# Kernel tuning notes

Measured on AMD Instinct MI355X. Metric: run time of the kernel, lower is better.

The kernel has to match this reference:

```python
import jax, jax.numpy as jnp
import numpy as np

N_HEAD = 16

def _apply_rotary(x, cos, sin):
    # x: (B,H,T,D); faithful to torch: x*cos + cat([-x[...,1::2], x[...,::2]], -1)*sin
    rot = jnp.concatenate([-x[..., 1::2], x[..., ::2]], axis=-1)
    return x * cos + rot * sin

def setup_inputs() -> dict:
    key = jax.random.key(0)
    k1, k2, k3 = jax.random.split(key, 3)
    B, T, C = 8, 1024, 1024
    x = jax.random.normal(k1, (B, T, C), dtype=jnp.float32)
    # scale weights like typical init to keep activations sane
    W_attn = jax.random.normal(k2, (3 * C, C), dtype=jnp.float32) * (C ** -0.5)
    W_proj = jax.random.normal(k3, (C, C), dtype=jnp.float32) * (C ** -0.5)
    return {"x": x, "W_attn": W_attn, "W_proj": W_proj}

def reference(x, W_attn, W_proj):
    B, T, C = x.shape
    H = N_HEAD
    D = C // H
    qkv = x @ W_attn.T                      # (B,T,3C)
    q, k, v = jnp.split(qkv, 3, axis=2)
    # (B,T,C) -> (B,H,T,D)
    def to_heads(t):
        return t.reshape(B, T, H, D).transpose(0, 2, 1, 3)
    q, k, v = to_heads(q), to_heads(k), to_heads(v)
    # Rotary module in source computes cos/sin of q itself (faithful reproduction)
    cos = jnp.cos(q)
    sin = jnp.sin(q)
    q = _apply_rotary(q, cos, sin)
    k = _apply_rotary(k, cos, sin)
    # causal attention, softmax_scale = 1.0 (as in the flash call)
    scores = jnp.einsum('bhqd,bhkd->bhqk', q, k)
    causal = jnp.tril(jnp.ones((T, T), dtype=bool))
    scores = jnp.where(causal, scores, jnp.finfo(scores.dtype).min)
    att = jax.nn.softmax(scores, axis=-1)
    y = jnp.einsum('bhqk,bhkd->bhqd', att, v)   # (B,H,T,D)
    y = y.transpose(0, 2, 1, 3).reshape(B, T, C)
    return y @ W_proj.T
```

## Files before the change

### kernel.cpp

```cpp
#include <hip/hip_runtime.h>

typedef __attribute__((ext_vector_type(8))) short v8s;
typedef __attribute__((ext_vector_type(8))) _Float16 f16x8;
typedef __attribute__((ext_vector_type(4))) _Float16 f16x4;
typedef __attribute__((ext_vector_type(4))) float f32x4;
typedef unsigned short u16;

#define MFMAH(a,b,c) __builtin_amdgcn_mfma_f32_16x16x32_f16((a),(b),(c),0,0,0)
#define L2E 1.4426950408889634f

__device__ __forceinline__ u16 f2h(float f) {
    _Float16 h = (_Float16)f;
    return __builtin_bit_cast(u16, h);
}

__device__ __forceinline__ void gload16(const u16* g, u16* l) {
    __builtin_amdgcn_global_load_lds((const __attribute__((address_space(1))) void*)g,
                                     (__attribute__((address_space(3))) void*)l, 16, 0, 0);
}

__device__ __forceinline__ void stage_tile(const u16* __restrict__ base, u16* lds, int w, int lane) {
    const int rsub = lane >> 3;
    const int s_org = (lane & 7) ^ rsub;
#pragma unroll
    for (int i = 0; i < 4; ++i) {
        const u16* src = base + (size_t)(32 * w + 8 * i + rsub) * 1024 + 8 * s_org;
        gload16(src, lds + (32 * w + 8 * i) * 64);
    }
}

__global__ __launch_bounds__(256) void split16_kernel(const float* __restrict__ in,
                                                      u16* __restrict__ hi, u16* __restrict__ lo, int n4) {
    int i = blockIdx.x * 256 + threadIdx.x;
    if (i >= n4) return;
    f32x4 v = ((const f32x4*)in)[i];
    f16x4 h, l;
#pragma unroll
    for (int j = 0; j < 4; ++j) {
        _Float16 hh = (_Float16)v[j];
        h[j] = hh;
        l[j] = (_Float16)(v[j] - (float)hh);
    }
    ((f16x4*)hi)[i] = h;
    ((f16x4*)lo)[i] = l;
}

__global__ __launch_bounds__(256) void cvt16_kernel(const float* __restrict__ in, u16* __restrict__ out, int n4) {
    int i = blockIdx.x * 256 + threadIdx.x;
    if (i >= n4) return;
    f32x4 v = ((const f32x4*)in)[i];
    f16x4 h;
#pragma unroll
    for (int j = 0; j < 4; ++j) h[j] = (_Float16)v[j];
    ((f16x4*)out)[i] = h;
}

__global__ __launch_bounds__(256) void qkv_gemm2(const u16* __restrict__ xh, const u16* __restrict__ xl,
                                                 const u16* __restrict__ wf, float* __restrict__ qkv) {
    __shared__ u16 sAh[8192], sAl[8192], sB[8192];
    const int bid = blockIdx.x;
    const int swz = (bid & 7) * 192 + (bid >> 3);
    const int mb = swz / 24, nb = swz % 24;
    const int m0 = mb * 128, n0 = nb * 128;
    const bool lo = (nb < 16);
    const int tid = threadIdx.x, lane = tid & 63, w = tid >> 6;
    const int wr = w >> 1, wc = w & 1;
    const int fr = lane & 15, fq = lane >> 4;
    const u16* pa = xh + (size_t)m0 * 1024;
    const u16* pal = xl + (size_t)m0 * 1024;
    const u16* pb = wf + (size_t)n0 * 1024;
    f32x4 acc[4][4] = {};
    for (int k0 = 0; k0 < 1024; k0 += 64) {
        stage_tile(pa + k0, sAh, w, lane);
        stage_tile(pb + k0, sB, w, lane);
        if (lo) stage_tile(pal + k0, sAl, w, lane);
        __syncthreads();
#pragma unroll
        for (int kk = 0; kk < 2; ++kk) {
            f16x8 ah[4], al[4], bb[4];
#pragma unroll
            for (int m = 0; m < 4; ++m) {
                int row = wr * 64 + m * 16 + fr;
                int off = row * 64 + ((((kk * 4 + fq)) ^ (fr & 7)) << 3);
                ah[m] = *(const f16x8*)&sAh[off];
                if (lo) al[m] = *(const f16x8*)&sAl[off];
            }
#pragma unroll
            for (int n = 0; n < 4; ++n) {
                int row = wc * 64 + n * 16 + fr;
                bb[n] = *(const f16x8*)&sB[row * 64 + ((((kk * 4 + fq)) ^ (fr & 7)) << 3)];
            }
#pragma unroll
            for (int n = 0; n < 4; ++n)
#pragma unroll
                for (int m = 0; m < 4; ++m) {
                    acc[m][n] = MFMAH(ah[m], bb[n], acc[m][n]);
                    if (lo) acc[m][n] = MFMAH(al[m], bb[n], acc[m][n]);
                }
        }
        __syncthreads();
    }
#pragma unroll
    for (int m = 0; m < 4; ++m) {
        int rowb = m0 + wr * 64 + m * 16 + fq * 4;
#pragma unroll
        for (int n = 0; n < 4; ++n) {
            int col = n0 + wc * 64 + n * 16 + fr;
#pragma unroll
            for (int r = 0; r < 4; ++r)
                qkv[(size_t)(rowb + r) * 3072 + col] = acc[m][n][r];
        }
    }
}

__global__ __launch_bounds__(256) void rotary_kernel(const float* __restrict__ qkv,
                                                     u16* __restrict__ qf, u16* __restrict__ kf,
                                                     u16* __restrict__ vt) {
    int rid = blockIdx.x * 4 + (threadIdx.x >> 6);
    int lane = threadIdx.x & 63;
    int b = rid >> 14, h = (rid >> 10) & 15, t = rid & 1023;
    const float* base = qkv + (size_t)(b * 1024 + t) * 3072 + h * 64 + lane;
    float q = base[0], k = base[1024], v = base[2048];
    float s, c;
    sincosf(q, &s, &c);
    int src = (lane < 32) ? (2 * lane + 1) : (2 * lane - 64);
    float qp = __shfl(q, src);
    float kp = __shfl(k, src);
    float rq = (lane < 32) ? -qp : qp;
    float rk = (lane < 32) ? -kp : kp;
    float q2 = q * c + rq * s;
    float k2 = k * c + rk * s;
    size_t oi = (size_t)((b * 16 + h) * 1024 + t) * 64 + lane;
    qf[oi] = f2h(q2);
    kf[oi] = f2h(k2);
    vt[(size_t)((b * 16 + h) * 64 + lane) * 1024 + t] = f2h(v);
}

__global__ __launch_bounds__(256) void attn_kernel(const u16* __restrict__ qf, const u16* __restrict__ kf,
                                                   const u16* __restrict__ vt, u16* __restrict__ yb) {
    __shared__ u16 sQ[4096], sK[4096], sV[4096], sP[4096];
    const int bh = blockIdx.x >> 4, qt = blockIdx.x & 15;
    const int b = bh >> 4, h = bh & 15;
    const int tid = threadIdx.x, lane = tid & 63, w = tid >> 6;
    const int q0 = qt * 64;
    const int fr = lane & 15, fq = lane >> 4;
    const int srow = tid >> 2, sc = (tid & 3) << 4;
    const int ss0 = sc >> 3;
    const int wr0 = srow * 64 + (((ss0    ) ^ (srow & 7)) << 3);
    const int wr1 = srow * 64 + (((ss0 + 1) ^ (srow & 7)) << 3);
    {
        const u16* g = qf + (size_t)(bh * 1024 + q0 + srow) * 64 + sc;
        *(v8s*)&sQ[wr0] = *(const v8s*)g;
        *(v8s*)&sQ[wr1] = *(const v8s*)(g + 8);
    }
    __syncthreads();
    f16x8 qfr[2];
    {
        int row = w * 16 + fr;
#pragma unroll
        for (int kk = 0; kk < 2; ++kk) {
            int sl = kk * 4 + fq;
            qfr[kk] = *(const f16x8*)&sQ[row * 64 + ((sl ^ (row & 7)) << 3)];
        }
    }
    f32x4 accy[4] = {};
    float m_r[4], l_r[4];
#pragma unroll
    for (int r = 0; r < 4; ++r) { m_r[r] = -1e30f; l_r[r] = 0.f; }
    const u16* gk = kf + (size_t)bh * 65536 + srow * 64 + sc;
    const u16* gv = vt + (size_t)(bh * 64 + srow) * 1024 + sc;

    for (int kt = 0; kt <= qt; ++kt) {
        __syncthreads();
        {
            const u16* a  = gk + kt * 4096;
            const u16* vg = gv + kt * 64;
            *(v8s*)&sK[wr0] = *(const v8s*)a;
            *(v8s*)&sK[wr1] = *(const v8s*)(a + 8);
            *(v8s*)&sV[wr0] = *(const v8s*)vg;
            *(v8s*)&sV[wr1] = *(const v8s*)(vg + 8);
        }
        __syncthreads();
        f32x4 s[4] = {};
#pragma unroll
        for (int n = 0; n < 4; ++n) {
            int krow = n * 16 + fr;
#pragma unroll
            for (int kk = 0; kk < 2; ++kk) {
                int sl = kk * 4 + fq;
                f16x8 kb = *(const f16x8*)&sK[krow * 64 + ((sl ^ (krow & 7)) << 3)];
                s[n] = MFMAH(qfr[kk], kb, s[n]);
            }
        }
        if (kt == qt) {
            int rowb = w * 16 + fq * 4;
#pragma unroll
            for (int n = 0; n < 4; ++n)
#pragma unroll
                for (int r = 0; r < 4; ++r)
                    if (n * 16 + fr > rowb + r) s[n][r] = -1e30f;
        }
        float alpha[4];
#pragma unroll
        for (int r = 0; r < 4; ++r) {
            float mx = fmaxf(fmaxf(s[0][r], s[1][r]), fmaxf(s[2][r], s[3][r]));
            mx = fmaxf(mx, __shfl_xor(mx, 1));
            mx = fmaxf(mx, __shfl_xor(mx, 2));
            mx = fmaxf(mx, __shfl_xor(mx, 4));
            mx = fmaxf(mx, __shfl_xor(mx, 8));
            float mn = fmaxf(m_r[r], mx);
            alpha[r] = exp2f((m_r[r] - mn) * L2E);
            m_r[r] = mn;
            float rs = 0.f;
#pragma unroll
            for (int n = 0; n < 4; ++n) {
                float p = exp2f((s[n][r] - mn) * L2E);
                s[n][r] = p;
                rs += p;
            }
            rs += __shfl_xor(rs, 1);
            rs += __shfl_xor(rs, 2);
            rs += __shfl_xor(rs, 4);
            rs += __shfl_xor(rs, 8);
            l_r[r] = l_r[r] * alpha[r] + rs;
        }
#pragma unroll
        for (int dn = 0; dn < 4; ++dn)
#pragma unroll
            for (int r = 0; r < 4; ++r) accy[dn][r] *= alpha[r];
        {
            int rowb = w * 16 + fq * 4;
#pragma unroll
            for (int n = 0; n < 4; ++n) {
                int key = n * 16 + fr;
                int s8 = key >> 3, kr = key & 7;
#pragma unroll
                for (int r = 0; r < 4; ++r) {
                    int row = rowb + r;
                    sP[row * 64 + (((s8 ^ (row & 7)) << 3) | kr)] = f2h(s[n][r]);
                }
            }
        }
        f16x8 pa[2];
        {
            int prow = w * 16 + fr;
#pragma unroll
            for (int kk = 0; kk < 2; ++kk) {
                int sl = kk * 4 + fq;
                pa[kk] = *(const f16x8*)&sP[prow * 64 + ((sl ^ (prow & 7)) << 3)];
            }
        }
#pragma unroll
        for (int dn = 0; dn < 4; ++dn) {
            int vrow = dn * 16 + fr;
#pragma unroll
            for (int kk = 0; kk < 2; ++kk) {
                int sl = kk * 4 + fq;
                f16x8 vb = *(const f16x8*)&sV[vrow * 64 + ((sl ^ (vrow & 7)) << 3)];
                accy[dn] = MFMAH(pa[kk], vb, accy[dn]);
            }
        }
    }
    {
        int rowb = q0 + w * 16 + fq * 4;
        int colb = h * 64 + fr;
#pragma unroll
        for (int r = 0; r < 4; ++r) {
            float inv = 1.0f / l_r[r];
#pragma unroll
            for (int dn = 0; dn < 4; ++dn)
                yb[(size_t)(b * 1024 + rowb + r) * 1024 + colb + dn * 16] = f2h(accy[dn][r] * inv);
        }
    }
}

__global__ __launch_bounds__(256) void proj_gemm2(const u16* __restrict__ yb, const u16* __restrict__ wpb,
                                                  float* __restrict__ out) {
    __shared__ u16 sA[8192], sB[8192];
    const int bid = blockIdx.x;
    const int swz = (bid & 7) * 64 + (bid >> 3);
    const int mb = swz >> 3, nb = swz & 7;
    const int m0 = mb * 128, n0 = nb * 128;
    const int tid = threadIdx.x, lane = tid & 63, w = tid >> 6;
    const int wr = w >> 1, wc = w & 1;
    const int fr = lane & 15, fq = lane >> 4;
    const u16* pa = yb + (size_t)m0 * 1024;
    const u16* pb = wpb + (size_t)n0 * 1024;
    f32x4 acc[4][4] = {};
    for (int k0 = 0; k0 < 1024; k0 += 64) {
        stage_tile(pa + k0, sA, w, lane);
        stage_tile(pb + k0, sB, w, lane);
        __syncthreads();
#pragma unroll
        for (int kk = 0; kk < 2; ++kk) {
            f16x8 af[4], bb[4];
#pragma unroll
            for (int m = 0; m < 4; ++m) {
                int row = wr * 64 + m * 16 + fr;
                af[m] = *(const f16x8*)&sA[row * 64 + ((((kk * 4 + fq)) ^ (fr & 7)) << 3)];
            }
#pragma unroll
            for (int n = 0; n < 4; ++n) {
                int row = wc * 64 + n * 16 + fr;
                bb[n] = *(const f16x8*)&sB[row * 64 + ((((kk * 4 + fq)) ^ (fr & 7)) << 3)];
            }
#pragma unroll
            for (int n = 0; n < 4; ++n)
#pragma unroll
                for (int m = 0; m < 4; ++m) acc[m][n] = MFMAH(af[m], bb[n], acc[m][n]);
        }
        __syncthreads();
    }
#pragma unroll
    for (int m = 0; m < 4; ++m) {
        int rowb = m0 + wr * 64 + m * 16 + fq * 4;
#pragma unroll
        for (int n = 0; n < 4; ++n) {
            int col = n0 + wc * 64 + n * 16 + fr;
#pragma unroll
            for (int r = 0; r < 4; ++r) out[(size_t)(rowb + r) * 1024 + col] = acc[m][n][r];
        }
    }
}

extern "C" void kernel_launch(void* const* d_in, const int* in_sizes, int n_in,
                              void* d_out, int out_size, void* d_ws, size_t ws_size,
                              hipStream_t stream) {
    const float* x  = (const float*)d_in[0];
    const float* Wa = (const float*)d_in[1];
    const float* Wp = (const float*)d_in[2];
    float* out = (float*)d_out;
    char* ws = (char*)d_ws;
    size_t off = 0;
    float* qkv = (float*)(ws + off); off += (size_t)8192 * 3072 * 4;
    u16* xh  = (u16*)(ws + off); off += 16777216;
    u16* xl  = (u16*)(ws + off); off += 16777216;
    u16* wf  = (u16*)(ws + off); off += 6291456;
    u16* wpb = (u16*)(ws + off); off += 2097152;
    u16* qf  = (u16*)(ws + off); off += 16777216;
    u16* kf  = (u16*)(ws + off); off += 16777216;
    u16* vt  = (u16*)(ws + off); off += 16777216;
    u16* yb  = (u16*)(ws + off); off += 16777216;

    split16_kernel<<<8192, 256, 0, stream>>>(x, xh, xl, 8192 * 1024 / 4);
    cvt16_kernel<<<3072, 256, 0, stream>>>(Wa, wf, 3072 * 1024 / 4);
    cvt16_kernel<<<1024, 256, 0, stream>>>(Wp, wpb, 1024 * 1024 / 4);
    qkv_gemm2<<<1536, 256, 0, stream>>>(xh, xl, wf, qkv);
    rotary_kernel<<<32768, 256, 0, stream>>>(qkv, qf, kf, vt);
    attn_kernel<<<2048, 256, 0, stream>>>(qf, kf, vt, yb);
    proj_gemm2<<<512, 256, 0, stream>>>(yb, wpb, out);
}
```

Measured before the change: 375.3 us.

## Pair causal query tiles per block to balance work and share K/V tiles

The attention kernel now gives each block two query tiles (qt and 15-qt), so every block runs the same number of key-tile iterations and each staged K/V tile serves both query tiles. Staging switches to async global_load_lds with a swizzled layout, the Q/P buffers are merged to cut shared memory, and launch bounds request 4 blocks per CU. The aim is to remove the load imbalance of the causal triangle and halve K/V reloads. In exchange the grid shrinks to 1024 blocks, the serial chain per block gets longer, and register pressure rises from two sets of accumulators.

```diff
diff --git a/kernel.cpp b/kernel.cpp
--- a/kernel.cpp
+++ b/kernel.cpp
@@ -26,6 +26,17 @@
     for (int i = 0; i < 4; ++i) {
         const u16* src = base + (size_t)(32 * w + 8 * i + rsub) * 1024 + 8 * s_org;
         gload16(src, lds + (32 * w + 8 * i) * 64);
+    }
+}
+
+__device__ __forceinline__ void stage64(const u16* __restrict__ base, size_t rstride,
+                                        u16* lds, int w, int lane) {
+    const int rsub = lane >> 3;
+    const int s_org = (lane & 7) ^ rsub;
+#pragma unroll
+    for (int i = 0; i < 2; ++i) {
+        const u16* src = base + (size_t)(16 * w + 8 * i + rsub) * rstride + 8 * s_org;
+        gload16(src, lds + (16 * w + 8 * i) * 64);
     }
 }
 
@@ -136,140 +147,144 @@
     vt[(size_t)((b * 16 + h) * 64 + lane) * 1024 + t] = f2h(v);
 }
 
-__global__ __launch_bounds__(256) void attn_kernel(const u16* __restrict__ qf, const u16* __restrict__ kf,
-                                                   const u16* __restrict__ vt, u16* __restrict__ yb) {
-    __shared__ u16 sQ[4096], sK[4096], sV[4096], sP[4096];
-    const int bh = blockIdx.x >> 4, qt = blockIdx.x & 15;
+__device__ __forceinline__ void attn_step(const f16x8* qfr, f32x4* accy, float* m_r, float* l_r,
+                                          const u16* sK, const u16* sV, u16* sP,
+                                          bool diag, int w, int lane) {
+    const int fr = lane & 15, fq = lane >> 4;
+    f32x4 s[4] = {};
+#pragma unroll
+    for (int n = 0; n < 4; ++n) {
+        int krow = n * 16 + fr;
+#pragma unroll
+        for (int kk = 0; kk < 2; ++kk) {
+            int sl = kk * 4 + fq;
+            f16x8 kb = *(const f16x8*)&sK[krow * 64 + ((sl ^ (krow & 7)) << 3)];
+            s[n] = MFMAH(qfr[kk], kb, s[n]);
+        }
+    }
+    if (diag) {
+        int rowb = w * 16 + fq * 4;
+#pragma unroll
+        for (int n = 0; n < 4; ++n)
+#pragma unroll
+            for (int r = 0; r < 4; ++r)
+                if (n * 16 + fr > rowb + r) s[n][r] = -1e30f;
+    }
+    float alpha[4];
+#pragma unroll
+    for (int r = 0; r < 4; ++r) {
+        float mx = fmaxf(fmaxf(s[0][r], s[1][r]), fmaxf(s[2][r], s[3][r]));
+        mx = fmaxf(mx, __shfl_xor(mx, 1));
+        mx = fmaxf(mx, __shfl_xor(mx, 2));
+        mx = fmaxf(mx, __shfl_xor(mx, 4));
+        mx = fmaxf(mx, __shfl_xor(mx, 8));
+        float mn = fmaxf(m_r[r], mx);
+        alpha[r] = exp2f((m_r[r] - mn) * L2E);
+        m_r[r] = mn;
+        float rs = 0.f;
+#pragma unroll
+        for (int n = 0; n < 4; ++n) {
+            float p = exp2f((s[n][r] - mn) * L2E);
+            s[n][r] = p;
+            rs += p;
+        }
+        rs += __shfl_xor(rs, 1);
+        rs += __shfl_xor(rs, 2);
+        rs += __shfl_xor(rs, 4);
+        rs += __shfl_xor(rs, 8);
+        l_r[r] = l_r[r] * alpha[r] + rs;
+    }
+#pragma unroll
+    for (int dn = 0; dn < 4; ++dn)
+#pragma unroll
+        for (int r = 0; r < 4; ++r) accy[dn][r] *= alpha[r];
+    {
+        int rowb = w * 16 + fq * 4;
+#pragma unroll
+        for (int n = 0; n < 4; ++n) {
+            int key = n * 16 + fr;
+            int s8 = key >> 3, kr = key & 7;
+#pragma unroll
+            for (int r = 0; r < 4; ++r) {
+                int row = rowb + r;
+                sP[row * 64 + (((s8 ^ (row & 7)) << 3) | kr)] = f2h(s[n][r]);
+            }
+        }
+    }
+    f16x8 pa[2];
+    {
+        int prow = w * 16 + fr;
+#pragma unroll
+        for (int kk = 0; kk < 2; ++kk) {
+            int sl = kk * 4 + fq;
+            pa[kk] = *(const f16x8*)&sP[prow * 64 + ((sl ^ (prow & 7)) << 3)];
+        }
+    }
+#pragma unroll
+    for (int dn = 0; dn < 4; ++dn) {
+        int vrow = dn * 16 + fr;
+#pragma unroll
+        for (int kk = 0; kk < 2; ++kk) {
+            int sl = kk * 4 + fq;
+            f16x8 vb = *(const f16x8*)&sV[vrow * 64 + ((sl ^ (vrow & 7)) << 3)];
+            accy[dn] = MFMAH(pa[kk], vb, accy[dn]);
+        }
+    }
+}
+
+__global__ __launch_bounds__(256, 4) void attn2_kernel(const u16* __restrict__ qf, const u16* __restrict__ kf,
+                                                       const u16* __restrict__ vt, u16* __restrict__ yb) {
+    __shared__ u16 sK[4096], sV[4096], sQP[4096];
+    const int bh = blockIdx.x >> 3, slot = blockIdx.x & 7;
     const int b = bh >> 4, h = bh & 15;
+    const int qtA = 15 - slot, qtB = slot;
     const int tid = threadIdx.x, lane = tid & 63, w = tid >> 6;
-    const int q0 = qt * 64;
     const int fr = lane & 15, fq = lane >> 4;
-    const int srow = tid >> 2, sc = (tid & 3) << 4;
-    const int ss0 = sc >> 3;
-    const int wr0 = srow * 64 + (((ss0    ) ^ (srow & 7)) << 3);
-    const int wr1 = srow * 64 + (((ss0 + 1) ^ (srow & 7)) << 3);
-    {
-        const u16* g = qf + (size_t)(bh * 1024 + q0 + srow) * 64 + sc;
-        *(v8s*)&sQ[wr0] = *(const v8s*)g;
-        *(v8s*)&sQ[wr1] = *(const v8s*)(g + 8);
-    }
+
+    stage64(qf + (size_t)bh * 65536 + qtA * 4096, 64, sK, w, lane);
+    stage64(qf + (size_t)bh * 65536 + qtB * 4096, 64, sV, w, lane);
     __syncthreads();
-    f16x8 qfr[2];
+    f16x8 qfrA[2], qfrB[2];
     {
         int row = w * 16 + fr;
 #pragma unroll
         for (int kk = 0; kk < 2; ++kk) {
             int sl = kk * 4 + fq;
-            qfr[kk] = *(const f16x8*)&sQ[row * 64 + ((sl ^ (row & 7)) << 3)];
-        }
-    }
-    f32x4 accy[4] = {};
-    float m_r[4], l_r[4];
-#pragma unroll
-    for (int r = 0; r < 4; ++r) { m_r[r] = -1e30f; l_r[r] = 0.f; }
-    const u16* gk = kf + (size_t)bh * 65536 + srow * 64 + sc;
-    const u16* gv = vt + (size_t)(bh * 64 + srow) * 1024 + sc;
-
-    for (int kt = 0; kt <= qt; ++kt) {
-        __syncthreads();
-        {
-            const u16* a  = gk + kt * 4096;
-            const u16* vg = gv + kt * 64;
-            *(v8s*)&sK[wr0] = *(const v8s*)a;
-            *(v8s*)&sK[wr1] = *(const v8s*)(a + 8);
-            *(v8s*)&sV[wr0] = *(const v8s*)vg;
-            *(v8s*)&sV[wr1] = *(const v8s*)(vg + 8);
-        }
-        __syncthreads();
-        f32x4 s[4] = {};
-#pragma unroll
-        for (int n = 0; n < 4; ++n) {
-            int krow = n * 16 + fr;
-#pragma unroll
-            for (int kk = 0; kk < 2; ++kk) {
-                int sl = kk * 4 + fq;
-                f16x8 kb = *(const f16x8*)&sK[krow * 64 + ((sl ^ (krow & 7)) << 3)];
-                s[n] = MFMAH(qfr[kk], kb, s[n]);
-            }
-        }
-        if (kt == qt) {
-            int rowb = w * 16 + fq * 4;
-#pragma unroll
-            for (int n = 0; n < 4; ++n)
-#pragma unroll
-                for (int r = 0; r < 4; ++r)
-                    if (n * 16 + fr > rowb + r) s[n][r] = -1e30f;
-        }
-        float alpha[4];
+            int off = row * 64 + ((sl ^ (row & 7)) << 3);
+            qfrA[kk] = *(const f16x8*)&sK[off];
+            qfrB[kk] = *(const f16x8*)&sV[off];
+        }
+    }
+    f32x4 accyA[4] = {}, accyB[4] = {};
+    float mA[4], lA[4], mB[4], lB[4];
+#pragma unroll
+    for (int r = 0; r < 4; ++r) { mA[r] = mB[r] = -1e30f; lA[r] = lB[r] = 0.f; }
+    const u16* kbase = kf + (size_t)bh * 65536;
+    const u16* vbase = vt + (size_t)bh * 65536;
+
+    for (int kt = 0; kt <= qtA; ++kt) {
+        __syncthreads();
+        stage64(kbase + kt * 4096, 64, sK, w, lane);
+        stage64(vbase + kt * 64, 1024, sV, w, lane);
+        __syncthreads();
+        attn_step(qfrA, accyA, mA, lA, sK, sV, sQP, kt == qtA, w, lane);
+        if (kt <= qtB)
+            attn_step(qfrB, accyB, mB, lB, sK, sV, sQP, kt == qtB, w, lane);
+    }
+    {
+        int rowbase = w * 16 + fq * 4;
+        int colb = h * 64 + fr;
 #pragma unroll
         for (int r = 0; r < 4; ++r) {
-            float mx = fmaxf(fmaxf(s[0][r], s[1][r]), fmaxf(s[2][r], s[3][r]));
-            mx = fmaxf(mx, __shfl_xor(mx, 1));
-            mx = fmaxf(mx, __shfl_xor(mx, 2));
-            mx = fmaxf(mx, __shfl_xor(mx, 4));
-            mx = fmaxf(mx, __shfl_xor(mx, 8));
-            float mn = fmaxf(m_r[r], mx);
-            alpha[r] = exp2f((m_r[r] - mn) * L2E);
-            m_r[r] = mn;
-            float rs = 0.f;
-#pragma unroll
-            for (int n = 0; n < 4; ++n) {
-                float p = exp2f((s[n][r] - mn) * L2E);
-                s[n][r] = p;
-                rs += p;
-            }
-            rs += __shfl_xor(rs, 1);
-            rs += __shfl_xor(rs, 2);
-            rs += __shfl_xor(rs, 4);
-            rs += __shfl_xor(rs, 8);
-            l_r[r] = l_r[r] * alpha[r] + rs;
-        }
-#pragma unroll
-        for (int dn = 0; dn < 4; ++dn)
-#pragma unroll
-            for (int r = 0; r < 4; ++r) accy[dn][r] *= alpha[r];
-        {
-            int rowb = w * 16 + fq * 4;
-#pragma unroll
-            for (int n = 0; n < 4; ++n) {
-                int key = n * 16 + fr;
-                int s8 = key >> 3, kr = key & 7;
-#pragma unroll
-                for (int r = 0; r < 4; ++r) {
-                    int row = rowb + r;
-                    sP[row * 64 + (((s8 ^ (row & 7)) << 3) | kr)] = f2h(s[n][r]);
-                }
-            }
-        }
-        f16x8 pa[2];
-        {
-            int prow = w * 16 + fr;
-#pragma unroll
-            for (int kk = 0; kk < 2; ++kk) {
-                int sl = kk * 4 + fq;
-                pa[kk] = *(const f16x8*)&sP[prow * 64 + ((sl ^ (prow & 7)) << 3)];
-            }
-        }
-#pragma unroll
-        for (int dn = 0; dn < 4; ++dn) {
-            int vrow = dn * 16 + fr;
-#pragma unroll
-            for (int kk = 0; kk < 2; ++kk) {
-                int sl = kk * 4 + fq;
-                f16x8 vb = *(const f16x8*)&sV[vrow * 64 + ((sl ^ (vrow & 7)) << 3)];
-                accy[dn] = MFMAH(pa[kk], vb, accy[dn]);
-            }
-        }
-    }
-    {
-        int rowb = q0 + w * 16 + fq * 4;
-        int colb = h * 64 + fr;
-#pragma unroll
-        for (int r = 0; r < 4; ++r) {
-            float inv = 1.0f / l_r[r];
-#pragma unroll
-            for (int dn = 0; dn < 4; ++dn)
-                yb[(size_t)(b * 1024 + rowb + r) * 1024 + colb + dn * 16] = f2h(accy[dn][r] * inv);
+            float invA = 1.0f / lA[r];
+            float invB = 1.0f / lB[r];
+            int rowA = qtA * 64 + rowbase + r;
+            int rowB = qtB * 64 + rowbase + r;
+#pragma unroll
+            for (int dn = 0; dn < 4; ++dn) {
+                yb[(size_t)(b * 1024 + rowA) * 1024 + colb + dn * 16] = f2h(accyA[dn][r] * invA);
+                yb[(size_t)(b * 1024 + rowB) * 1024 + colb + dn * 16] = f2h(accyB[dn][r] * invB);
+            }
         }
     }
 }
@@ -347,6 +362,6 @@
     cvt16_kernel<<<1024, 256, 0, stream>>>(Wp, wpb, 1024 * 1024 / 4);
     qkv_gemm2<<<1536, 256, 0, stream>>>(xh, xl, wf, qkv);
     rotary_kernel<<<32768, 256, 0, stream>>>(qkv, qf, kf, vt);
-    attn_kernel<<<2048, 256, 0, stream>>>(qf, kf, vt, yb);
+    attn2_kernel<<<1024, 256, 0, stream>>>(qf, kf, vt, yb);
     proj_gemm2<<<512, 256, 0, stream>>>(yb, wpb, out);
 }
```

Measured after the change: 463.7 us. 23.6% more time.
